# Kernel tuning notes

Hardware: AMD Instinct MI355X
Metric: run time of the kernel (lower is better)

## Reference

```python
import jax, jax.numpy as jnp
import numpy as np

D_MODEL = 384
KSIZE = 3
B, L = 32, 512
LN_EPS = 1e-5


def _conv1d_same(x, w, b):
    # x: [B, C_in, L], w: [C_out, C_in, K] -> [B, C_out, L]
    y = jax.lax.conv_general_dilated(
        x, w, window_strides=(1,), padding='SAME',
        dimension_numbers=('NCH', 'OIH', 'NCH'))
    return y + b[None, :, None]


def _conv_fft_block(x, wa, ba, wb, bb):
    # Conv1D_FFT: transpose -> conv/relu -> conv/relu -> transpose back
    h = jnp.transpose(x, (0, 2, 1))            # [B, D, L]
    h = jax.nn.relu(_conv1d_same(h, wa, ba))
    h = jax.nn.relu(_conv1d_same(h, wb, bb))
    return jnp.transpose(h, (0, 2, 1))         # [B, L, D]


def _layernorm(x, g, b):
    mu = jnp.mean(x, axis=-1, keepdims=True)
    var = jnp.var(x, axis=-1, keepdims=True)
    return (x - mu) * jax.lax.rsqrt(var + LN_EPS) * g + b


def setup_inputs() -> dict:
    key = jax.random.key(0)
    ks = jax.random.split(key, 8)
    x = jax.random.normal(ks[0], (B, L, D_MODEL), dtype=jnp.float32)
    durations = jax.random.randint(ks[1], (B, L), 0, 8, dtype=jnp.int32)
    s = 0.02
    params = {
        'c1a_w': jax.random.normal(ks[2], (D_MODEL, D_MODEL, KSIZE), jnp.float32) * s,
        'c1a_b': jnp.zeros((D_MODEL,), jnp.float32),
        'c1b_w': jax.random.normal(ks[3], (D_MODEL, D_MODEL, KSIZE), jnp.float32) * s,
        'c1b_b': jnp.zeros((D_MODEL,), jnp.float32),
        'ln1_g': jnp.ones((D_MODEL,), jnp.float32),
        'ln1_b': jnp.zeros((D_MODEL,), jnp.float32),
        'c2a_w': jax.random.normal(ks[4], (D_MODEL, D_MODEL, KSIZE), jnp.float32) * s,
        'c2a_b': jnp.zeros((D_MODEL,), jnp.float32),
        'c2b_w': jax.random.normal(ks[5], (D_MODEL, D_MODEL, KSIZE), jnp.float32) * s,
        'c2b_b': jnp.zeros((D_MODEL,), jnp.float32),
        'ln2_g': jnp.ones((D_MODEL,), jnp.float32),
        'ln2_b': jnp.zeros((D_MODEL,), jnp.float32),
        'lin_w': jax.random.normal(ks[6], (D_MODEL, 1), jnp.float32) * s,
        'lin_b': jnp.zeros((1,), jnp.float32),
    }
    return {'x': x, 'durations': durations, **params}


def reference(x, durations, c1a_w, c1a_b, c1b_w, c1b_b, ln1_g, ln1_b,
              c2a_w, c2a_b, c2b_w, c2b_b, ln2_g, ln2_b, lin_w, lin_b):
    # --- DurationPredictor (dropout = identity, eval mode) ---
    h = _conv_fft_block(x, c1a_w, c1a_b, c1b_w, c1b_b)
    h = _layernorm(h, ln1_g, ln1_b)
    h = _conv_fft_block(h, c2a_w, c2a_b, c2b_w, c2b_b)
    h = _layernorm(h, ln2_g, ln2_b)
    dur_preds = (h @ lin_w + lin_b)[..., 0]      # [B, L]

    # --- LR: duration-based expansion via one-hot alignment matmul ---
    total = jnp.sum(durations, axis=-1)          # [B]
    T = int(jnp.max(total))                      # concrete (durations are input data)
    cum = jnp.cumsum(durations, axis=-1)         # [B, L]
    t = jnp.arange(T, dtype=cum.dtype)           # [T]
    # frame t belongs to phoneme j s.t. cum[j-1] <= t < cum[j]
    idx = jax.vmap(lambda c: jnp.searchsorted(c, t, side='right'))(cum)  # [B, T]
    mask = (t[None, :] < total[:, None]).astype(x.dtype)                 # [B, T]
    align = jax.nn.one_hot(idx, x.shape[1], dtype=x.dtype) * mask[:, :, None]  # [B, T, L]
    out = jnp.einsum('btl,bld->btd', align, x)   # [B, T, D]
    return (out, dur_preds)
```

## Files before the change

### kernel.cpp

```cpp
#include <hip/hip_runtime.h>

#define B_   32
#define L_   512
#define D_   384
#define M_   (B_*L_)
#define KTOT (D_*3)
#define LDW  392
#define BROWS 82
#define BUFE (BROWS*LDW)

typedef __bf16 bf16x8 __attribute__((ext_vector_type(8)));
typedef float  floatx4 __attribute__((ext_vector_type(4)));

__global__ __launch_bounds__(256) void repack4_kernel(const float* __restrict__ wa,
                                                      const float* __restrict__ wb,
                                                      const float* __restrict__ wc,
                                                      const float* __restrict__ wd,
                                                      __bf16* __restrict__ oa,
                                                      __bf16* __restrict__ ob,
                                                      __bf16* __restrict__ oc,
                                                      __bf16* __restrict__ od)
{
    int idx = blockIdx.x * 256 + threadIdx.x;
    if (idx >= D_ * KTOT) return;
    const float* w; __bf16* o_;
    switch (blockIdx.y) {
        case 0:  w = wa; o_ = oa; break;
        case 1:  w = wb; o_ = ob; break;
        case 2:  w = wc; o_ = oc; break;
        default: w = wd; o_ = od; break;
    }
    int j  = idx & 7;
    int l  = (idx >> 3) & 63;
    int ct = idx >> 9;
    int c  = ct / 24;
    int t  = ct - c * 24;
    int o  = t * 16 + (l & 15);
    int kflat = c * 32 + (l >> 4) * 8 + j;
    int s  = kflat / D_;
    int i  = kflat - s * D_;
    o_[idx] = (__bf16)w[(o * D_ + i) * 3 + s];
}

__global__ __launch_bounds__(512, 1) void fused_predictor(
    const float* __restrict__ x,
    const __bf16* __restrict__ w1a, const float* __restrict__ b1a,
    const __bf16* __restrict__ w1b, const float* __restrict__ b1b,
    const float* __restrict__ g1,  const float* __restrict__ e1,
    const __bf16* __restrict__ w2a, const float* __restrict__ b2a,
    const __bf16* __restrict__ w2b, const float* __restrict__ b2b,
    const float* __restrict__ g2,  const float* __restrict__ e2,
    const float* __restrict__ lw,  const float* __restrict__ lb,
    float* __restrict__ out_dur)
{
    extern __shared__ char smem_raw[];
    __bf16* bufA = (__bf16*)smem_raw;
    __bf16* bufB = bufA + BUFE;
    float*  red1 = (float*)(bufB + BUFE);
    float*  red2 = red1 + BROWS * 8;
    float*  minv = red2 + BROWS * 8;

    const int m0 = blockIdx.x * 64;
    const int l0 = m0 & 511;
    const int b0 = m0 - l0;

    const int tid  = threadIdx.x;
    const int wave = tid >> 6;
    const int lane = tid & 63;
    const int quad = lane >> 4;
    const int lx   = lane & 15;

    bf16x8 kz;
#pragma unroll
    for (int z = 0; z < 8; z++) kz[z] = (__bf16)0.f;

    for (int c = tid; c < BROWS * 48; c += 512) {
        int beta = c / 48, q = c - beta * 48;
        int l = l0 + beta - 9;
        bf16x8 v = kz;
        if ((unsigned)l < (unsigned)L_) {
            const float* xr = x + (size_t)(b0 + l) * D_ + q * 8;
            const float4 f0 = *(const float4*)xr;
            const float4 f1 = *(const float4*)(xr + 4);
            v[0] = (__bf16)f0.x; v[1] = (__bf16)f0.y; v[2] = (__bf16)f0.z; v[3] = (__bf16)f0.w;
            v[4] = (__bf16)f1.x; v[5] = (__bf16)f1.y; v[6] = (__bf16)f1.z; v[7] = (__bf16)f1.w;
        }
        *(bf16x8*)(&bufA[beta * LDW + q * 8]) = v;
    }
    for (int c = tid; c < 2 * 48; c += 512) {
        int beta = (c < 48) ? 0 : 81, q = c % 48;
        *(bf16x8*)(&bufB[beta * LDW + q * 8]) = kz;
    }
    __syncthreads();

    const int t0  = wave * 3;
    const int col0 = wave * 48 + lx;

    floatx4 acc[5][3];
    bf16x8  bg[3][3];

    for (int st = 0; st < 4; st++) {
        const __bf16* bin  = (st & 1) ? bufB : bufA;
        __bf16*       bout = (st & 1) ? bufA : bufB;
        const __bf16* Wp = (st == 0) ? w1a : (st == 1) ? w1b : (st == 2) ? w2a : w2b;
        const float*  bp = (st == 0) ? b1a : (st == 1) ? b1b : (st == 2) ? b2a : b2b;

#pragma unroll
        for (int mt = 0; mt < 5; mt++)
#pragma unroll
            for (int ni = 0; ni < 3; ni++)
#pragma unroll
                for (int r = 0; r < 4; r++) acc[mt][ni][r] = 0.f;

        const char* pb0 = (const char*)Wp + ((size_t)t0 * 64 + lane) * 16;
        auto loadB = [&](int buf, int n) {
            int it = n / 3, s = n - it * 3;
            const char* p = pb0 + (size_t)(s * 12 + it) * 24576;
#pragma unroll
            for (int ni = 0; ni < 3; ni++)
                bg[buf][ni] = *(const bf16x8*)(p + ni * 1024);
        };
        loadB(0, 0); loadB(1, 1);

        const __bf16* ab = bin + lx * LDW + quad * 8;
#pragma unroll
        for (int n = 0; n < 36; n++) {
            const int it = n / 3, s = n - it * 3;
            if (n + 2 < 36) loadB((n + 2) % 3, n + 2);
            bf16x8 af[5];
#pragma unroll
            for (int mt = 0; mt < 5; mt++)
                af[mt] = *(const bf16x8*)(ab + (mt * 16 + s) * LDW + it * 32);
#pragma unroll
            for (int mt = 0; mt < 5; mt++)
#pragma unroll
                for (int ni = 0; ni < 3; ni++)
                    acc[mt][ni] = __builtin_amdgcn_mfma_f32_16x16x32_bf16(af[mt], bg[n % 3][ni], acc[mt][ni], 0, 0, 0);
        }

        float bv[3];
#pragma unroll
        for (int ni = 0; ni < 3; ni++) bv[ni] = bp[col0 + ni * 16];
#pragma unroll
        for (int mt = 0; mt < 5; mt++)
#pragma unroll
            for (int ni = 0; ni < 3; ni++)
#pragma unroll
                for (int r = 0; r < 4; r++) {
                    float vv = acc[mt][ni][r] + bv[ni];
                    acc[mt][ni][r] = vv > 0.f ? vv : 0.f;
                }

        if (st == 1 || st == 3) {
#pragma unroll
            for (int mt = 0; mt < 5; mt++)
#pragma unroll
                for (int r = 0; r < 4; r++) {
                    float s1 = acc[mt][0][r] + acc[mt][1][r] + acc[mt][2][r];
                    float s2 = acc[mt][0][r] * acc[mt][0][r] + acc[mt][1][r] * acc[mt][1][r]
                             + acc[mt][2][r] * acc[mt][2][r];
#pragma unroll
                    for (int d = 1; d < 16; d <<= 1) {
                        s1 += __shfl_xor(s1, d);
                        s2 += __shfl_xor(s2, d);
                    }
                    if (lx == 0) {
                        int beta = mt * 16 + quad * 4 + r + 1;
                        red1[beta * 8 + wave] = s1;
                        red2[beta * 8 + wave] = s2;
                    }
                }
            __syncthreads();
            if (tid < BROWS) {
                float s1 = 0.f, s2 = 0.f;
#pragma unroll
                for (int w = 0; w < 8; w++) { s1 += red1[tid * 8 + w]; s2 += red2[tid * 8 + w]; }
                float mean = s1 * (1.f / D_);
                float var  = s2 * (1.f / D_) - mean * mean;
                minv[tid * 2]     = mean;
                minv[tid * 2 + 1] = rsqrtf(var + 1e-5f);
            }
            __syncthreads();
            const float* gp = (st == 1) ? g1 : g2;
            const float* ep = (st == 1) ? e1 : e2;
            float gv[3], ev[3];
#pragma unroll
            for (int ni = 0; ni < 3; ni++) { gv[ni] = gp[col0 + ni * 16]; ev[ni] = ep[col0 + ni * 16]; }
#pragma unroll
            for (int mt = 0; mt < 5; mt++)
#pragma unroll
                for (int r = 0; r < 4; r++) {
                    int beta = mt * 16 + quad * 4 + r + 1;
                    float mean = minv[beta * 2], inv = minv[beta * 2 + 1];
#pragma unroll
                    for (int ni = 0; ni < 3; ni++)
                        acc[mt][ni][r] = (acc[mt][ni][r] - mean) * inv * gv[ni] + ev[ni];
                }
            if (st == 1) {
#pragma unroll
                for (int mt = 0; mt < 5; mt++)
#pragma unroll
                    for (int r = 0; r < 4; r++) {
                        int beta = mt * 16 + quad * 4 + r + 1;
                        bool ok = (unsigned)(l0 + beta - 9) < (unsigned)L_;
#pragma unroll
                        for (int ni = 0; ni < 3; ni++)
                            bout[beta * LDW + col0 + ni * 16] = (__bf16)(ok ? acc[mt][ni][r] : 0.f);
                    }
            } else {
                float lwv[3];
#pragma unroll
                for (int ni = 0; ni < 3; ni++) lwv[ni] = lw[col0 + ni * 16];
#pragma unroll
                for (int mt = 0; mt < 5; mt++)
#pragma unroll
                    for (int r = 0; r < 4; r++) {
                        float p = acc[mt][0][r] * lwv[0] + acc[mt][1][r] * lwv[1] + acc[mt][2][r] * lwv[2];
#pragma unroll
                        for (int d = 1; d < 16; d <<= 1) p += __shfl_xor(p, d);
                        if (lx == 0) {
                            int beta = mt * 16 + quad * 4 + r + 1;
                            red1[beta * 8 + wave] = p;
                        }
                    }
                __syncthreads();
                if (tid < 64) {
                    int beta = tid + 9;
                    float sacc = lb[0];
#pragma unroll
                    for (int w = 0; w < 8; w++) sacc += red1[beta * 8 + w];
                    out_dur[m0 + tid] = sacc;
                }
            }
        } else {
#pragma unroll
            for (int mt = 0; mt < 5; mt++)
#pragma unroll
                for (int r = 0; r < 4; r++) {
                    int beta = mt * 16 + quad * 4 + r + 1;
                    bool ok = (unsigned)(l0 + beta - 9) < (unsigned)L_;
#pragma unroll
                    for (int ni = 0; ni < 3; ni++)
                        bout[beta * LDW + col0 + ni * 16] = (__bf16)(ok ? acc[mt][ni][r] : 0.f);
                }
        }
        __syncthreads();
    }
}

__global__ __launch_bounds__(64) void cum_kernel(const int* __restrict__ dur,
                                                 int* __restrict__ cum)
{
    int b = blockIdx.x, lane = threadIdx.x;
    const int* db = dur + b * L_;
    int v[8], s = 0;
#pragma unroll
    for (int i = 0; i < 8; i++) { v[i] = db[lane * 8 + i]; s += v[i]; }
    int ex = s;
#pragma unroll
    for (int off = 1; off < 64; off <<= 1) {
        int n = __shfl_up(ex, off);
        if (lane >= off) ex += n;
    }
    ex -= s;
    int c = ex;
    int* cb = cum + b * L_;
#pragma unroll
    for (int i = 0; i < 8; i++) { c += v[i]; cb[lane * 8 + i] = c; }
}

__global__ __launch_bounds__(128) void gather_kernel(const float* __restrict__ x,
                                                     const int* __restrict__ cum,
                                                     float* __restrict__ out, int T)
{
    int fr = blockIdx.x;
    int b  = fr / T;
    int t  = fr - b * T;
    int tid = threadIdx.x;
    const int* cb = cum + b * L_;
    int total = cb[L_ - 1];
    float4 val = make_float4(0.f, 0.f, 0.f, 0.f);
    if (t < total) {
        int lo = 0, hi = L_;
        while (lo < hi) { int mid = (lo + hi) >> 1; if (cb[mid] > t) hi = mid; else lo = mid + 1; }
        if (tid < 96) val = *(const float4*)(x + ((size_t)(b * L_ + lo)) * D_ + tid * 4);
    }
    if (tid < 96) *(float4*)(out + (size_t)fr * D_ + tid * 4) = val;
}

extern "C" void kernel_launch(void* const* d_in, const int* in_sizes, int n_in,
                              void* d_out, int out_size, void* d_ws, size_t ws_size,
                              hipStream_t stream) {
    const float* x       = (const float*)d_in[0];
    const int*   dur     = (const int*)d_in[1];
    const float* c1a_w   = (const float*)d_in[2];
    const float* c1a_b   = (const float*)d_in[3];
    const float* c1b_w   = (const float*)d_in[4];
    const float* c1b_b   = (const float*)d_in[5];
    const float* ln1_g   = (const float*)d_in[6];
    const float* ln1_b   = (const float*)d_in[7];
    const float* c2a_w   = (const float*)d_in[8];
    const float* c2a_b   = (const float*)d_in[9];
    const float* c2b_w   = (const float*)d_in[10];
    const float* c2b_b   = (const float*)d_in[11];
    const float* ln2_g   = (const float*)d_in[12];
    const float* ln2_b   = (const float*)d_in[13];
    const float* lin_w   = (const float*)d_in[14];
    const float* lin_b   = (const float*)d_in[15];

    const int T = (out_size - B_ * L_) / (B_ * D_);
    float* out_gather = (float*)d_out;
    float* out_dur    = (float*)d_out + (size_t)B_ * T * D_;

    char* p = (char*)d_ws;
    __bf16* w1a = (__bf16*)p; p += (size_t)D_ * KTOT * 2;
    __bf16* w1b = (__bf16*)p; p += (size_t)D_ * KTOT * 2;
    __bf16* w2a = (__bf16*)p; p += (size_t)D_ * KTOT * 2;
    __bf16* w2b = (__bf16*)p; p += (size_t)D_ * KTOT * 2;
    int* cum = (int*)p; p += (size_t)B_ * L_ * 4;

    cum_kernel<<<B_, 64, 0, stream>>>(dur, cum);
    gather_kernel<<<B_ * T, 128, 0, stream>>>(x, cum, out_gather, T);

    dim3 rpgrid((D_ * KTOT + 255) / 256, 4);
    repack4_kernel<<<rpgrid, 256, 0, stream>>>(c1a_w, c1b_w, c2a_w, c2b_w, w1a, w1b, w2a, w2b);

    const size_t smem = (size_t)2 * BUFE * 2 + (BROWS * 8 * 2 + BROWS * 2) * 4;
    static bool attr_set = false;
    if (!attr_set) {
        hipFuncSetAttribute((const void*)fused_predictor,
                            hipFuncAttributeMaxDynamicSharedMemorySize, (int)smem);
        attr_set = true;
    }
    fused_predictor<<<256, 512, smem, stream>>>(
        x, w1a, c1a_b, w1b, c1b_b, ln1_g, ln1_b,
        w2a, c2a_b, w2b, c2b_b, ln2_g, ln2_b,
        lin_w, lin_b, out_dur);
}
```

Measured before the change: 253.9 us.

## XOR-swizzle LDS activation buffers and split gather into index and copy kernels

```diff
diff --git a/kernel.cpp b/kernel.cpp
--- a/kernel.cpp
+++ b/kernel.cpp
@@ -5,7 +5,7 @@
 #define D_   384
 #define M_   (B_*L_)
 #define KTOT (D_*3)
-#define LDW  392
+#define LDW  384
 #define BROWS 82
 #define BUFE (BROWS*LDW)
 
@@ -85,11 +85,11 @@
             v[0] = (__bf16)f0.x; v[1] = (__bf16)f0.y; v[2] = (__bf16)f0.z; v[3] = (__bf16)f0.w;
             v[4] = (__bf16)f1.x; v[5] = (__bf16)f1.y; v[6] = (__bf16)f1.z; v[7] = (__bf16)f1.w;
         }
-        *(bf16x8*)(&bufA[beta * LDW + q * 8]) = v;
+        *(bf16x8*)(&bufA[beta * LDW + ((q ^ (beta & 7)) << 3)]) = v;
     }
     for (int c = tid; c < 2 * 48; c += 512) {
         int beta = (c < 48) ? 0 : 81, q = c % 48;
-        *(bf16x8*)(&bufB[beta * LDW + q * 8]) = kz;
+        *(bf16x8*)(&bufB[beta * LDW + (q << 3)]) = kz;
     }
     __syncthreads();
 
@@ -122,15 +122,17 @@
         };
         loadB(0, 0); loadB(1, 1);
 
-        const __bf16* ab = bin + lx * LDW + quad * 8;
 #pragma unroll
         for (int n = 0; n < 36; n++) {
             const int it = n / 3, s = n - it * 3;
             if (n + 2 < 36) loadB((n + 2) % 3, n + 2);
+            const int key = (lx + s) & 7;
             bf16x8 af[5];
 #pragma unroll
-            for (int mt = 0; mt < 5; mt++)
-                af[mt] = *(const bf16x8*)(ab + (mt * 16 + s) * LDW + it * 32);
+            for (int mt = 0; mt < 5; mt++) {
+                const int beta = mt * 16 + s + lx;
+                af[mt] = *(const bf16x8*)(&bin[beta * LDW + (((it * 4 + quad) ^ key) << 3)]);
+            }
 #pragma unroll
             for (int mt = 0; mt < 5; mt++)
 #pragma unroll
@@ -202,10 +204,14 @@
 #pragma unroll
                     for (int r = 0; r < 4; r++) {
                         int beta = mt * 16 + quad * 4 + r + 1;
+                        int key = beta & 7;
                         bool ok = (unsigned)(l0 + beta - 9) < (unsigned)L_;
 #pragma unroll
-                        for (int ni = 0; ni < 3; ni++)
-                            bout[beta * LDW + col0 + ni * 16] = (__bf16)(ok ? acc[mt][ni][r] : 0.f);
+                        for (int ni = 0; ni < 3; ni++) {
+                            int col = col0 + ni * 16;
+                            bout[beta * LDW + ((((col >> 3) ^ key) << 3) | (col & 7))] =
+                                (__bf16)(ok ? acc[mt][ni][r] : 0.f);
+                        }
                     }
             } else {
                 float lwv[3];
@@ -238,10 +244,14 @@
 #pragma unroll
                 for (int r = 0; r < 4; r++) {
                     int beta = mt * 16 + quad * 4 + r + 1;
+                    int key = beta & 7;
                     bool ok = (unsigned)(l0 + beta - 9) < (unsigned)L_;
 #pragma unroll
-                    for (int ni = 0; ni < 3; ni++)
-                        bout[beta * LDW + col0 + ni * 16] = (__bf16)(ok ? acc[mt][ni][r] : 0.f);
+                    for (int ni = 0; ni < 3; ni++) {
+                        int col = col0 + ni * 16;
+                        bout[beta * LDW + ((((col >> 3) ^ key) << 3) | (col & 7))] =
+                            (__bf16)(ok ? acc[mt][ni][r] : 0.f);
+                    }
                 }
         }
         __syncthreads();
@@ -269,23 +279,35 @@
     for (int i = 0; i < 8; i++) { c += v[i]; cb[lane * 8 + i] = c; }
 }
 
-__global__ __launch_bounds__(128) void gather_kernel(const float* __restrict__ x,
-                                                     const int* __restrict__ cum,
-                                                     float* __restrict__ out, int T)
-{
-    int fr = blockIdx.x;
-    int b  = fr / T;
-    int t  = fr - b * T;
-    int tid = threadIdx.x;
+__global__ __launch_bounds__(256) void idx_kernel(const int* __restrict__ cum,
+                                                  int* __restrict__ idx, int T, int nf)
+{
+    int f = blockIdx.x * 256 + threadIdx.x;
+    if (f >= nf) return;
+    int b = f / T;
+    int t = f - b * T;
     const int* cb = cum + b * L_;
-    int total = cb[L_ - 1];
-    float4 val = make_float4(0.f, 0.f, 0.f, 0.f);
-    if (t < total) {
+    int v = -1;
+    if (t < cb[L_ - 1]) {
         int lo = 0, hi = L_;
         while (lo < hi) { int mid = (lo + hi) >> 1; if (cb[mid] > t) hi = mid; else lo = mid + 1; }
-        if (tid < 96) val = *(const float4*)(x + ((size_t)(b * L_ + lo)) * D_ + tid * 4);
-    }
-    if (tid < 96) *(float4*)(out + (size_t)fr * D_ + tid * 4) = val;
+        v = b * L_ + lo;
+    }
+    idx[f] = v;
+}
+
+__global__ __launch_bounds__(256) void copy_kernel(const float* __restrict__ x,
+                                                   const int* __restrict__ idx,
+                                                   float* __restrict__ out, int nchunks)
+{
+    int gid = blockIdx.x * 256 + threadIdx.x;
+    if (gid >= nchunks) return;
+    int f = gid / 96;
+    int c = gid - f * 96;
+    int src = idx[f];
+    float4 v = make_float4(0.f, 0.f, 0.f, 0.f);
+    if (src >= 0) v = *(const float4*)(x + (size_t)src * D_ + c * 4);
+    *(float4*)(out + (size_t)gid * 4) = v;
 }
 
 extern "C" void kernel_launch(void* const* d_in, const int* in_sizes, int n_in,
@@ -318,20 +340,20 @@
     __bf16* w2a = (__bf16*)p; p += (size_t)D_ * KTOT * 2;
     __bf16* w2b = (__bf16*)p; p += (size_t)D_ * KTOT * 2;
     int* cum = (int*)p; p += (size_t)B_ * L_ * 4;
-
+    int* idx = (int*)p; p += (size_t)B_ * T * 4;
+
+    const int nf = B_ * T;
     cum_kernel<<<B_, 64, 0, stream>>>(dur, cum);
-    gather_kernel<<<B_ * T, 128, 0, stream>>>(x, cum, out_gather, T);
+    idx_kernel<<<(nf + 255) / 256, 256, 0, stream>>>(cum, idx, T, nf);
+    const int nchunks = nf * 96;
+    copy_kernel<<<(nchunks + 255) / 256, 256, 0, stream>>>(x, idx, out_gather, nchunks);
 
     dim3 rpgrid((D_ * KTOT + 255) / 256, 4);
     repack4_kernel<<<rpgrid, 256, 0, stream>>>(c1a_w, c1b_w, c2a_w, c2b_w, w1a, w1b, w2a, w2b);
 
     const size_t smem = (size_t)2 * BUFE * 2 + (BROWS * 8 * 2 + BROWS * 2) * 4;
-    static bool attr_set = false;
-    if (!attr_set) {
-        hipFuncSetAttribute((const void*)fused_predictor,
-                            hipFuncAttributeMaxDynamicSharedMemorySize, (int)smem);
-        attr_set = true;
-    }
+    hipFuncSetAttribute((const void*)fused_predictor,
+                        hipFuncAttributeMaxDynamicSharedMemorySize, (int)smem);
     fused_predictor<<<256, 512, smem, stream>>>(
         x, w1a, c1a_b, w1b, c1b_b, ln1_g, ln1_b,
         w2a, c2a_b, w2b, c2b_b, ln2_g, ln2_b,
```

Measured after the change: 306.9 us. 20.9% more time.
